# Optimization experiments

Hardware: AMD Instinct MI355X
Metric: run time of the kernel (lower is better)

The kernel has to match this reference:

```python
import jax, jax.numpy as jnp
import numpy as np

N_NODES = 50000
N_EDGES = 1600000
N_EDGE_F = 128
GLOBAL_F = 64
N_GRAPHS = 512
HIDDEN = N_EDGE_F // 2


def setup_inputs() -> dict:
    key = jax.random.key(0)
    k = jax.random.split(key, 8)
    x = jax.random.normal(k[0], (N_NODES, N_EDGE_F), dtype=jnp.float32)
    edge_index = jax.random.randint(k[1], (2, N_EDGES), 0, N_NODES, dtype=jnp.int64)
    edge_attr = jax.random.normal(k[2], (N_EDGES, N_EDGE_F), dtype=jnp.float32)
    u = jax.random.normal(k[3], (N_GRAPHS, GLOBAL_F), dtype=jnp.float32)
    batch = jnp.sort(jax.random.randint(k[4], (N_NODES,), 0, N_GRAPHS, dtype=jnp.int64))
    # MLP params (Linear1: in=n_edge_f+global_f, out=hidden; Linear2: hidden -> global_f)
    in1 = N_EDGE_F + GLOBAL_F
    W1 = jax.random.normal(k[5], (in1, HIDDEN), dtype=jnp.float32) / np.sqrt(in1)
    b1 = jnp.zeros((HIDDEN,), dtype=jnp.float32)
    W2 = jax.random.normal(k[6], (HIDDEN, GLOBAL_F), dtype=jnp.float32) / np.sqrt(HIDDEN)
    b2 = jnp.zeros((GLOBAL_F,), dtype=jnp.float32)
    return {"x": x, "edge_index": edge_index, "edge_attr": edge_attr, "u": u,
            "batch": batch, "W1": W1, "b1": b1, "W2": W2, "b2": b2}


def reference(x, edge_index, edge_attr, u, batch, W1, b1, W2, b2):
    # graph id of each edge = graph id of its source node
    seg = batch[edge_index[0]]                                   # [E]
    sums = jax.ops.segment_sum(edge_attr, seg, num_segments=N_GRAPHS)  # [B, n_edge_f]
    counts = jax.ops.segment_sum(jnp.ones((edge_attr.shape[0],), edge_attr.dtype),
                                 seg, num_segments=N_GRAPHS)
    mean = sums / jnp.maximum(counts, 1.0)[:, None]              # scatter-mean (0 for empty)
    out = jnp.concatenate([u, mean], axis=1)                     # [B, global_f + n_edge_f]
    # dropout in eval mode == identity
    h = jax.nn.relu(out @ W1 + b1)
    return h @ W2 + b2
```

## Files before the change

### kernel.cpp

```cpp
#include <hip/hip_runtime.h>
#include <hip/hip_bf16.h>

typedef unsigned int u32;
typedef unsigned short u16;
typedef float f32x4 __attribute__((ext_vector_type(4)));

#define NGR   512
#define NF    128
#define GF    64
#define HID   64
#define IN1   192
#define CHUNK 1024
#define MAXIT 2600

#define HT    256
#define ITEMS 10
#define EPB   (HT * ITEMS)

__global__ void zero_counts_kernel(u32* __restrict__ counts) {
    counts[threadIdx.x] = 0u;
}

__global__ void hist_kernel(const int* __restrict__ ei0,
                            const int* __restrict__ batch,
                            u32* __restrict__ g_counts,
                            u16* __restrict__ seg, int E) {
    __shared__ u32 h[NGR];
    int tid = threadIdx.x;
    h[tid] = 0u; h[tid + 256] = 0u;
    __syncthreads();
    int base = blockIdx.x * EPB + tid;
#pragma unroll
    for (int i = 0; i < ITEMS; ++i) {
        int e = base + i * HT;
        if (e < E) {
            int s = batch[ei0[e]];
            seg[e] = (u16)s;
            atomicAdd(&h[s], 1u);
        }
    }
    __syncthreads();
    u32 v0 = h[tid];       if (v0) atomicAdd(&g_counts[tid], v0);
    u32 v1 = h[tid + 256]; if (v1) atomicAdd(&g_counts[tid + 256], v1);
}

__global__ void scan_kernel(const u32* __restrict__ counts,
                            u32* __restrict__ offsets,
                            u32* __restrict__ cursor,
                            u32* __restrict__ work,
                            u32* __restrict__ item_start,
                            u32* __restrict__ header) {
    __shared__ u32 A[NGR], B[NGR];
    int t = threadIdx.x;
    u32 c = counts[t];
    A[t] = c;
    __syncthreads();
    u32 *src = A, *dst = B;
    for (int off = 1; off < NGR; off <<= 1) {
        u32 v = src[t];
        if (t >= off) v += src[t - off];
        dst[t] = v;
        __syncthreads();
        u32* tmp = src; src = dst; dst = tmp;
    }
    u32 exc = src[t] - c;
    offsets[t] = exc;
    cursor[t]  = exc;
    __syncthreads();
    u32 ns = (c + CHUNK - 1) / CHUNK;
    A[t] = ns;
    __syncthreads();
    src = A; dst = B;
    for (int off = 1; off < NGR; off <<= 1) {
        u32 v = src[t];
        if (t >= off) v += src[t - off];
        dst[t] = v;
        __syncthreads();
        u32* tmp = src; src = dst; dst = tmp;
    }
    u32 istart = src[t] - ns;
    item_start[t] = istart;
    if (t == NGR - 1) { item_start[NGR] = istart + ns; header[0] = istart + ns; }
    for (u32 s = 0; s < ns; ++s) work[istart + s] = ((u32)t << 16) | s;
}

__global__ void scatter_kernel(const u16* __restrict__ seg,
                               u32* __restrict__ cursor,
                               u32* __restrict__ sorted, int E) {
    __shared__ u32 h[NGR];
    __shared__ u32 bs[NGR];
    int tid = threadIdx.x;
    h[tid] = 0u; h[tid + 256] = 0u;
    __syncthreads();
    int base = blockIdx.x * EPB + tid;
    u16 segs[ITEMS];
    u16 ranks[ITEMS];
#pragma unroll
    for (int i = 0; i < ITEMS; ++i) {
        int e = base + i * HT;
        if (e < E) {
            int s = seg[e];
            segs[i]  = (u16)s;
            ranks[i] = (u16)atomicAdd(&h[s], 1u);
        }
    }
    __syncthreads();
    u32 v0 = h[tid];       if (v0) bs[tid]       = atomicAdd(&cursor[tid], v0);
    u32 v1 = h[tid + 256]; if (v1) bs[tid + 256] = atomicAdd(&cursor[tid + 256], v1);
    __syncthreads();
#pragma unroll
    for (int i = 0; i < ITEMS; ++i) {
        int e = base + i * HT;
        if (e < E) sorted[bs[segs[i]] + ranks[i]] = (u32)e;
    }
}

__launch_bounds__(256, 8)
__global__ void reduce_kernel(const float* __restrict__ edge_attr,
                              const u32* __restrict__ sorted,
                              const u32* __restrict__ counts,
                              const u32* __restrict__ offsets,
                              const u32* __restrict__ work,
                              const u32* __restrict__ header,
                              float* __restrict__ partial) {
    const u32 id = blockIdx.x;
    if (id >= header[0]) return;
    __shared__ float red[8 * NF];

    const u32 w = work[id];
    const int g = (int)(w >> 16);
    const u32 sl = w & 0xFFFFu;
    const u32 off = offsets[g] + sl * CHUNK;
    const u32 len = min((u32)CHUNK, counts[g] - sl * CHUNK);

    const int tid = threadIdx.x;
    const int row = tid >> 5;
    const int lane = tid & 31;

    f32x4 a0 = {0.f,0.f,0.f,0.f}, a1 = a0, a2 = a0, a3 = a0;

    u32 j = (u32)row;
    for (; j + 24 < len; j += 32) {
        u32 e0 = sorted[off + j];
        u32 e1 = sorted[off + j + 8];
        u32 e2 = sorted[off + j + 16];
        u32 e3 = sorted[off + j + 24];
        f32x4 v0 = __builtin_nontemporal_load((const f32x4*)(edge_attr + (size_t)e0 * NF) + lane);
        f32x4 v1 = __builtin_nontemporal_load((const f32x4*)(edge_attr + (size_t)e1 * NF) + lane);
        f32x4 v2 = __builtin_nontemporal_load((const f32x4*)(edge_attr + (size_t)e2 * NF) + lane);
        f32x4 v3 = __builtin_nontemporal_load((const f32x4*)(edge_attr + (size_t)e3 * NF) + lane);
        a0 += v0; a1 += v1; a2 += v2; a3 += v3;
    }
    for (; j < len; j += 8) {
        u32 e = sorted[off + j];
        f32x4 v = __builtin_nontemporal_load((const f32x4*)(edge_attr + (size_t)e * NF) + lane);
        a0 += v;
    }
    a0 += a1 + a2 + a3;
    *(f32x4*)(red + row * NF + lane * 4) = a0;
    __syncthreads();

    if (tid < NF) {
        float s = 0.f;
#pragma unroll
        for (int r = 0; r < 8; ++r) s += red[r * NF + tid];
        partial[(size_t)id * NF + tid] = s;
    }
}

__global__ void final_kernel(const float* __restrict__ partial,
                             const u32* __restrict__ counts,
                             const u32* __restrict__ item_start,
                             const float* __restrict__ u,
                             const float* __restrict__ W1,
                             const float* __restrict__ b1,
                             const float* __restrict__ W2,
                             const float* __restrict__ b2,
                             float* __restrict__ out) {
    __shared__ float vin[IN1];
    __shared__ float hv[HID];
    const int g = blockIdx.x, t = threadIdx.x;
    const u32 a = item_start[g], b = item_start[g + 1];
    if (t < NF) {
        float s = 0.f;
        for (u32 it = a; it < b; ++it) s += partial[(size_t)it * NF + t];
        vin[GF + t] = s / fmaxf((float)counts[g], 1.0f);
    }
    if (t >= NF && t < NF + GF) vin[t - NF] = u[g * GF + (t - NF)];
    __syncthreads();
    if (t < HID) {
        float acc = b1[t];
#pragma unroll
        for (int k = 0; k < IN1; ++k) acc += vin[k] * W1[k * HID + t];
        hv[t] = fmaxf(acc, 0.0f);
    }
    __syncthreads();
    if (t < GF) {
        float acc = b2[t];
#pragma unroll
        for (int k = 0; k < HID; ++k) acc += hv[k] * W2[k * GF + t];
        out[g * GF + t] = acc;
    }
}

extern "C" void kernel_launch(void* const* d_in, const int* in_sizes, int n_in,
                              void* d_out, int out_size, void* d_ws, size_t ws_size,
                              hipStream_t stream) {
    const int*   ei        = (const int*)d_in[1];
    const float* edge_attr = (const float*)d_in[2];
    const float* u         = (const float*)d_in[3];
    const int*   batch     = (const int*)d_in[4];
    const float* W1        = (const float*)d_in[5];
    const float* b1        = (const float*)d_in[6];
    const float* W2        = (const float*)d_in[7];
    const float* b2        = (const float*)d_in[8];
    float*       out       = (float*)d_out;

    const int E = in_sizes[1] / 2;
    const int* ei0 = ei;

    u32*   sorted     = (u32*)d_ws;
    float* partial    = (float*)(sorted + E);
    u32*   counts     = (u32*)(partial + (size_t)MAXIT * NF);
    u32*   offsets    = counts + NGR;
    u32*   cursor     = offsets + NGR;
    u32*   item_start = cursor + NGR;
    u32*   header     = item_start + NGR + 1;
    u32*   work       = header + 16;
    u16*   seg        = (u16*)(work + MAXIT);

    const int nblocks = (E + EPB - 1) / EPB;

    zero_counts_kernel<<<1, NGR, 0, stream>>>(counts);
    hist_kernel<<<nblocks, HT, 0, stream>>>(ei0, batch, counts, seg, E);
    scan_kernel<<<1, NGR, 0, stream>>>(counts, offsets, cursor, work, item_start, header);
    scatter_kernel<<<nblocks, HT, 0, stream>>>(seg, cursor, sorted, E);
    reduce_kernel<<<MAXIT, 256, 0, stream>>>(edge_attr, sorted, counts, offsets,
                                             work, header, partial);
    final_kernel<<<NGR, 256, 0, stream>>>(partial, counts, item_start,
                                          u, W1, b1, W2, b2, out);
}
```

Baseline: 208.5 us.

## Fuse all stages into one cooperative kernel with grid syncs and dynamic work tickets

Replaces the six separate launches (zero, histogram, scan, scatter, reduce, final MLP) with a single cooperative kernel that separates phases with grid-wide syncs. Segment ids and ranks stay in registers between histogram and scatter, so the seg buffer round trip is gone. The reduce phase takes chunks of 256 edges from an atomic ticket queue instead of fixed 1024-edge blocks. This removes launch gaps and some memory traffic, but adds several grid.sync barriers and requires all ~625 blocks to be co-resident. The scan now runs inside one 256-thread block.

```diff
diff --git a/kernel.cpp b/kernel.cpp
--- a/kernel.cpp
+++ b/kernel.cpp
@@ -1,5 +1,8 @@
 #include <hip/hip_runtime.h>
+#include <hip/hip_cooperative_groups.h>
 #include <hip/hip_bf16.h>
+
+namespace cg = cooperative_groups;
 
 typedef unsigned int u32;
 typedef unsigned short u16;
@@ -10,196 +13,181 @@
 #define GF    64
 #define HID   64
 #define IN1   192
-#define CHUNK 1024
-#define MAXIT 2600
-
 #define HT    256
 #define ITEMS 10
 #define EPB   (HT * ITEMS)
-
-__global__ void zero_counts_kernel(u32* __restrict__ counts) {
-    counts[threadIdx.x] = 0u;
-}
-
-__global__ void hist_kernel(const int* __restrict__ ei0,
-                            const int* __restrict__ batch,
-                            u32* __restrict__ g_counts,
-                            u16* __restrict__ seg, int E) {
-    __shared__ u32 h[NGR];
-    int tid = threadIdx.x;
-    h[tid] = 0u; h[tid + 256] = 0u;
-    __syncthreads();
-    int base = blockIdx.x * EPB + tid;
-#pragma unroll
-    for (int i = 0; i < ITEMS; ++i) {
-        int e = base + i * HT;
-        if (e < E) {
-            int s = batch[ei0[e]];
-            seg[e] = (u16)s;
-            atomicAdd(&h[s], 1u);
-        }
-    }
-    __syncthreads();
-    u32 v0 = h[tid];       if (v0) atomicAdd(&g_counts[tid], v0);
-    u32 v1 = h[tid + 256]; if (v1) atomicAdd(&g_counts[tid + 256], v1);
-}
-
-__global__ void scan_kernel(const u32* __restrict__ counts,
-                            u32* __restrict__ offsets,
-                            u32* __restrict__ cursor,
-                            u32* __restrict__ work,
-                            u32* __restrict__ item_start,
-                            u32* __restrict__ header) {
-    __shared__ u32 A[NGR], B[NGR];
-    int t = threadIdx.x;
-    u32 c = counts[t];
-    A[t] = c;
-    __syncthreads();
-    u32 *src = A, *dst = B;
-    for (int off = 1; off < NGR; off <<= 1) {
-        u32 v = src[t];
-        if (t >= off) v += src[t - off];
-        dst[t] = v;
-        __syncthreads();
-        u32* tmp = src; src = dst; dst = tmp;
-    }
-    u32 exc = src[t] - c;
-    offsets[t] = exc;
-    cursor[t]  = exc;
-    __syncthreads();
-    u32 ns = (c + CHUNK - 1) / CHUNK;
-    A[t] = ns;
-    __syncthreads();
-    src = A; dst = B;
-    for (int off = 1; off < NGR; off <<= 1) {
-        u32 v = src[t];
-        if (t >= off) v += src[t - off];
-        dst[t] = v;
-        __syncthreads();
-        u32* tmp = src; src = dst; dst = tmp;
-    }
-    u32 istart = src[t] - ns;
-    item_start[t] = istart;
-    if (t == NGR - 1) { item_start[NGR] = istart + ns; header[0] = istart + ns; }
-    for (u32 s = 0; s < ns; ++s) work[istart + s] = ((u32)t << 16) | s;
-}
-
-__global__ void scatter_kernel(const u16* __restrict__ seg,
-                               u32* __restrict__ cursor,
-                               u32* __restrict__ sorted, int E) {
-    __shared__ u32 h[NGR];
-    __shared__ u32 bs[NGR];
-    int tid = threadIdx.x;
-    h[tid] = 0u; h[tid + 256] = 0u;
-    __syncthreads();
-    int base = blockIdx.x * EPB + tid;
-    u16 segs[ITEMS];
-    u16 ranks[ITEMS];
-#pragma unroll
-    for (int i = 0; i < ITEMS; ++i) {
-        int e = base + i * HT;
-        if (e < E) {
-            int s = seg[e];
-            segs[i]  = (u16)s;
-            ranks[i] = (u16)atomicAdd(&h[s], 1u);
-        }
-    }
-    __syncthreads();
-    u32 v0 = h[tid];       if (v0) bs[tid]       = atomicAdd(&cursor[tid], v0);
-    u32 v1 = h[tid + 256]; if (v1) bs[tid + 256] = atomicAdd(&cursor[tid + 256], v1);
-    __syncthreads();
-#pragma unroll
-    for (int i = 0; i < ITEMS; ++i) {
-        int e = base + i * HT;
-        if (e < E) sorted[bs[segs[i]] + ranks[i]] = (u32)e;
-    }
-}
-
-__launch_bounds__(256, 8)
-__global__ void reduce_kernel(const float* __restrict__ edge_attr,
-                              const u32* __restrict__ sorted,
-                              const u32* __restrict__ counts,
-                              const u32* __restrict__ offsets,
-                              const u32* __restrict__ work,
-                              const u32* __restrict__ header,
-                              float* __restrict__ partial) {
-    const u32 id = blockIdx.x;
-    if (id >= header[0]) return;
-    __shared__ float red[8 * NF];
-
-    const u32 w = work[id];
-    const int g = (int)(w >> 16);
-    const u32 sl = w & 0xFFFFu;
-    const u32 off = offsets[g] + sl * CHUNK;
-    const u32 len = min((u32)CHUNK, counts[g] - sl * CHUNK);
-
-    const int tid = threadIdx.x;
-    const int row = tid >> 5;
-    const int lane = tid & 31;
-
-    f32x4 a0 = {0.f,0.f,0.f,0.f}, a1 = a0, a2 = a0, a3 = a0;
-
-    u32 j = (u32)row;
-    for (; j + 24 < len; j += 32) {
-        u32 e0 = sorted[off + j];
-        u32 e1 = sorted[off + j + 8];
-        u32 e2 = sorted[off + j + 16];
-        u32 e3 = sorted[off + j + 24];
-        f32x4 v0 = __builtin_nontemporal_load((const f32x4*)(edge_attr + (size_t)e0 * NF) + lane);
-        f32x4 v1 = __builtin_nontemporal_load((const f32x4*)(edge_attr + (size_t)e1 * NF) + lane);
-        f32x4 v2 = __builtin_nontemporal_load((const f32x4*)(edge_attr + (size_t)e2 * NF) + lane);
-        f32x4 v3 = __builtin_nontemporal_load((const f32x4*)(edge_attr + (size_t)e3 * NF) + lane);
-        a0 += v0; a1 += v1; a2 += v2; a3 += v3;
-    }
-    for (; j < len; j += 8) {
-        u32 e = sorted[off + j];
-        f32x4 v = __builtin_nontemporal_load((const f32x4*)(edge_attr + (size_t)e * NF) + lane);
-        a0 += v;
-    }
-    a0 += a1 + a2 + a3;
-    *(f32x4*)(red + row * NF + lane * 4) = a0;
-    __syncthreads();
-
-    if (tid < NF) {
-        float s = 0.f;
-#pragma unroll
-        for (int r = 0; r < 8; ++r) s += red[r * NF + tid];
-        partial[(size_t)id * NF + tid] = s;
-    }
-}
-
-__global__ void final_kernel(const float* __restrict__ partial,
-                             const u32* __restrict__ counts,
-                             const u32* __restrict__ item_start,
+#define CH    256
+#define MAXIT 7000
+
+__launch_bounds__(256, 3)
+__global__ void fused_kernel(const float* __restrict__ edge_attr,
+                             const int* __restrict__ ei0,
+                             const int* __restrict__ batch,
                              const float* __restrict__ u,
                              const float* __restrict__ W1,
                              const float* __restrict__ b1,
                              const float* __restrict__ W2,
                              const float* __restrict__ b2,
-                             float* __restrict__ out) {
-    __shared__ float vin[IN1];
-    __shared__ float hv[HID];
-    const int g = blockIdx.x, t = threadIdx.x;
-    const u32 a = item_start[g], b = item_start[g + 1];
-    if (t < NF) {
-        float s = 0.f;
-        for (u32 it = a; it < b; ++it) s += partial[(size_t)it * NF + t];
-        vin[GF + t] = s / fmaxf((float)counts[g], 1.0f);
-    }
-    if (t >= NF && t < NF + GF) vin[t - NF] = u[g * GF + (t - NF)];
+                             float* __restrict__ out,
+                             u32* __restrict__ counts,
+                             u32* __restrict__ offsets,
+                             u32* __restrict__ cursor,
+                             u32* __restrict__ item_start,
+                             u32* __restrict__ header,
+                             u32* __restrict__ work,
+                             u32* __restrict__ sorted,
+                             float* __restrict__ partial,
+                             int E) {
+    cg::grid_group grid = cg::this_grid();
+    __shared__ u32 h[NGR];
+    __shared__ u32 bs[NGR];
+    __shared__ u32 AB[2 * NGR];
+    __shared__ u32 sh_item;
+
+    const int tid = threadIdx.x;
+    const int bid = blockIdx.x;
+
+    if (bid == 0) {
+        counts[tid] = 0u; counts[tid + 256] = 0u;
+        if (tid == 0) header[1] = 0u;
+    }
+    grid.sync();
+
+    h[tid] = 0u; h[tid + 256] = 0u;
     __syncthreads();
-    if (t < HID) {
-        float acc = b1[t];
-#pragma unroll
-        for (int k = 0; k < IN1; ++k) acc += vin[k] * W1[k * HID + t];
-        hv[t] = fmaxf(acc, 0.0f);
+    u16 segs[ITEMS], ranks[ITEMS];
+    const int base = bid * EPB + tid;
+#pragma unroll
+    for (int i = 0; i < ITEMS; ++i) {
+        int e = base + i * HT;
+        if (e < E) {
+            int s = batch[ei0[e]];
+            segs[i]  = (u16)s;
+            ranks[i] = (u16)atomicAdd(&h[s], 1u);
+        }
     }
     __syncthreads();
-    if (t < GF) {
-        float acc = b2[t];
-#pragma unroll
-        for (int k = 0; k < HID; ++k) acc += hv[k] * W2[k * GF + t];
-        out[g * GF + t] = acc;
+    { u32 v0 = h[tid];       if (v0) atomicAdd(&counts[tid], v0);
+      u32 v1 = h[tid + 256]; if (v1) atomicAdd(&counts[tid + 256], v1); }
+    grid.sync();
+
+    if (bid == 0) {
+        u32* A = AB; u32* Bb = AB + NGR;
+        u32 c0 = counts[tid], c1 = counts[tid + 256];
+        A[tid] = c0; A[tid + 256] = c1;
+        __syncthreads();
+        u32 *src = A, *dst = Bb;
+        for (int off = 1; off < NGR; off <<= 1) {
+            u32 v0 = src[tid];       if (tid >= off)       v0 += src[tid - off];
+            u32 v1 = src[tid + 256]; if (tid + 256 >= off) v1 += src[tid + 256 - off];
+            dst[tid] = v0; dst[tid + 256] = v1;
+            __syncthreads();
+            u32* tmp = src; src = dst; dst = tmp;
+        }
+        u32 e0 = src[tid] - c0, e1 = src[tid + 256] - c1;
+        offsets[tid] = e0;       cursor[tid] = e0;
+        offsets[tid + 256] = e1; cursor[tid + 256] = e1;
+        __syncthreads();
+        u32 n0 = (c0 + CH - 1) / CH, n1 = (c1 + CH - 1) / CH;
+        A[tid] = n0; A[tid + 256] = n1;
+        __syncthreads();
+        src = A; dst = Bb;
+        for (int off = 1; off < NGR; off <<= 1) {
+            u32 v0 = src[tid];       if (tid >= off)       v0 += src[tid - off];
+            u32 v1 = src[tid + 256]; if (tid + 256 >= off) v1 += src[tid + 256 - off];
+            dst[tid] = v0; dst[tid + 256] = v1;
+            __syncthreads();
+            u32* tmp = src; src = dst; dst = tmp;
+        }
+        u32 i0 = src[tid] - n0, i1 = src[tid + 256] - n1;
+        item_start[tid] = i0; item_start[tid + 256] = i1;
+        if (tid == 255) { item_start[NGR] = i1 + n1; header[0] = i1 + n1; }
+        for (u32 s = 0; s < n0; ++s) work[i0 + s] = ((u32)tid << 16) | s;
+        for (u32 s = 0; s < n1; ++s) work[i1 + s] = ((u32)(tid + 256) << 16) | s;
+    }
+    grid.sync();
+
+    { u32 v0 = h[tid];       if (v0) bs[tid]       = atomicAdd(&cursor[tid], v0);
+      u32 v1 = h[tid + 256]; if (v1) bs[tid + 256] = atomicAdd(&cursor[tid + 256], v1); }
+    __syncthreads();
+#pragma unroll
+    for (int i = 0; i < ITEMS; ++i) {
+        int e = base + i * HT;
+        if (e < E) sorted[bs[segs[i]] + ranks[i]] = (u32)e;
+    }
+    grid.sync();
+
+    {
+        float* red = (float*)AB;
+        const u32 nitems = header[0];
+        u32* ticket = header + 1;
+        const int row = tid >> 5, lane = tid & 31;
+        for (;;) {
+            __syncthreads();
+            if (tid == 0) sh_item = atomicAdd(ticket, 1u);
+            __syncthreads();
+            const u32 it = sh_item;
+            if (it >= nitems) break;
+            const u32 w = work[it];
+            const int g = (int)(w >> 16);
+            const u32 sl = w & 0xFFFFu;
+            const u32 off = offsets[g] + sl * CH;
+            const u32 len = min((u32)CH, counts[g] - sl * CH);
+
+            f32x4 a0 = {0.f,0.f,0.f,0.f}, a1 = a0, a2 = a0, a3 = a0;
+            u32 j = (u32)row;
+            for (; j + 24 < len; j += 32) {
+                u32 e0 = sorted[off + j];
+                u32 e1 = sorted[off + j + 8];
+                u32 e2 = sorted[off + j + 16];
+                u32 e3 = sorted[off + j + 24];
+                a0 += __builtin_nontemporal_load((const f32x4*)(edge_attr + (size_t)e0 * NF) + lane);
+                a1 += __builtin_nontemporal_load((const f32x4*)(edge_attr + (size_t)e1 * NF) + lane);
+                a2 += __builtin_nontemporal_load((const f32x4*)(edge_attr + (size_t)e2 * NF) + lane);
+                a3 += __builtin_nontemporal_load((const f32x4*)(edge_attr + (size_t)e3 * NF) + lane);
+            }
+            for (; j < len; j += 8) {
+                u32 e = sorted[off + j];
+                a0 += __builtin_nontemporal_load((const f32x4*)(edge_attr + (size_t)e * NF) + lane);
+            }
+            a0 += a1 + a2 + a3;
+            *(f32x4*)(red + row * NF + lane * 4) = a0;
+            __syncthreads();
+            if (tid < NF) {
+                float s = 0.f;
+#pragma unroll
+                for (int r = 0; r < 8; ++r) s += red[r * NF + tid];
+                partial[(size_t)it * NF + tid] = s;
+            }
+        }
+    }
+    grid.sync();
+
+    if (bid < NGR) {
+        const int g = bid;
+        float* vin = (float*)h;
+        float* hv  = (float*)bs;
+        const u32 a = item_start[g], b = item_start[g + 1];
+        if (tid < NF) {
+            float s = 0.f;
+            for (u32 it = a; it < b; ++it) s += partial[(size_t)it * NF + tid];
+            vin[GF + tid] = s / fmaxf((float)counts[g], 1.0f);
+        }
+        if (tid >= NF && tid < NF + GF) vin[tid - NF] = u[g * GF + (tid - NF)];
+        __syncthreads();
+        if (tid < HID) {
+            float acc = b1[tid];
+#pragma unroll
+            for (int k = 0; k < IN1; ++k) acc += vin[k] * W1[k * HID + tid];
+            hv[tid] = fmaxf(acc, 0.0f);
+        }
+        __syncthreads();
+        if (tid < GF) {
+            float acc = b2[tid];
+#pragma unroll
+            for (int k = 0; k < HID; ++k) acc += hv[k] * W2[k * GF + tid];
+            out[g * GF + tid] = acc;
+        }
     }
 }
 
@@ -216,7 +204,7 @@
     const float* b2        = (const float*)d_in[8];
     float*       out       = (float*)d_out;
 
-    const int E = in_sizes[1] / 2;
+    int E = in_sizes[1] / 2;
     const int* ei0 = ei;
 
     u32*   sorted     = (u32*)d_ws;
@@ -226,17 +214,17 @@
     u32*   cursor     = offsets + NGR;
     u32*   item_start = cursor + NGR;
     u32*   header     = item_start + NGR + 1;
-    u32*   work       = header + 16;
-    u16*   seg        = (u16*)(work + MAXIT);
-
-    const int nblocks = (E + EPB - 1) / EPB;
-
-    zero_counts_kernel<<<1, NGR, 0, stream>>>(counts);
-    hist_kernel<<<nblocks, HT, 0, stream>>>(ei0, batch, counts, seg, E);
-    scan_kernel<<<1, NGR, 0, stream>>>(counts, offsets, cursor, work, item_start, header);
-    scatter_kernel<<<nblocks, HT, 0, stream>>>(seg, cursor, sorted, E);
-    reduce_kernel<<<MAXIT, 256, 0, stream>>>(edge_attr, sorted, counts, offsets,
-                                             work, header, partial);
-    final_kernel<<<NGR, 256, 0, stream>>>(partial, counts, item_start,
-                                          u, W1, b1, W2, b2, out);
+    u32*   work       = header + 8;
+
+    const int nblk = (E + EPB - 1) / EPB;
+
+    void* args[] = {
+        (void*)&edge_attr, (void*)&ei0, (void*)&batch, (void*)&u,
+        (void*)&W1, (void*)&b1, (void*)&W2, (void*)&b2, (void*)&out,
+        (void*)&counts, (void*)&offsets, (void*)&cursor, (void*)&item_start,
+        (void*)&header, (void*)&work, (void*)&sorted, (void*)&partial,
+        (void*)&E
+    };
+    hipLaunchCooperativeKernel((const void*)fused_kernel, dim3(nblk), dim3(256),
+                               args, 0, stream);
 }
```

Result: slower. 573.8 us (+175.1%).
